# Optimization experiments

Measured on AMD Instinct MI355X. Metric: run time of the kernel, lower is better.

Reference implementation:

```python
import math
import jax, jax.numpy as jnp
import numpy as np

B, N, D, H, PQ, PV = 2, 2048, 256, 8, 4, 8
HD = D // H
OUT_IN = D + H * PV * 3 + H  # 256 + 192 + 8 = 456


def setup_inputs() -> dict:
    key = jax.random.key(0)
    ks = jax.random.split(key, 12)
    w = lambda k, shape: (jax.random.normal(k, shape, jnp.float32) * 0.02)
    return {
        "x": jax.random.normal(ks[0], (B, N, D), jnp.float32),
        "rotations": jax.random.normal(ks[1], (B, N, 3, 3), jnp.float32),
        "translations": jax.random.normal(ks[2], (B, N, 3), jnp.float32),
        "mask": jnp.ones((B, N), dtype=bool),
        "Wq": w(ks[3], (D, D)), "bq": jnp.zeros((D,), jnp.float32),
        "Wk": w(ks[4], (D, D)), "bk": jnp.zeros((D,), jnp.float32),
        "Wv": w(ks[5], (D, D)), "bv": jnp.zeros((D,), jnp.float32),
        "Wo": w(ks[6], (OUT_IN, D)), "bo": jnp.zeros((D,), jnp.float32),
        "head_weights": jnp.ones((H,), jnp.float32),
    }


def reference(x, rotations, translations, mask, Wq, bq, Wk, bk, Wv, bv, Wo, bo, head_weights):
    b, n, d = x.shape
    h = head_weights.shape[0]
    hd = d // h
    pv3 = Wo.shape[0] - d - h  # num_heads * num_value_points * 3

    q = (x @ Wq + bq).reshape(b, n, h, hd)
    k = (x @ Wk + bk).reshape(b, n, h, hd)
    v = (x @ Wv + bv).reshape(b, n, h, hd)

    # scalar attention logits [b,h,i,j]
    attn_scores = jnp.einsum("bihd,bjhd->bhij", q, k) / math.sqrt(hd)

    # point-distance bias from frame translations (rotated q/k/v points are
    # dead code in the original module and are omitted)
    diff = translations[:, :, None, :] - translations[:, None, :, :]  # [b,i,j,3]
    dist_sq = jnp.sum(diff * diff, axis=-1)                            # [b,i,j]
    point_attn = -0.5 * dist_sq[:, None, :, :]                         # [b,1,i,j]

    weights = jax.nn.softmax(head_weights)                             # [h]
    combined = attn_scores + point_attn * weights[None, :, None, None]
    combined = jnp.where(mask[:, None, None, :], combined, -1e9)
    attn_probs = jax.nn.softmax(combined, axis=-1)                     # [b,h,i,j]

    attn_output = jnp.einsum("bhij,bjhd->bihd", attn_probs, v).reshape(b, n, d)

    # translation-weighted points, brought back to local frame
    trans_weighted = jnp.einsum("bhij,bjc->bihc", attn_probs, translations)  # [b,i,h,3]
    trans_local = trans_weighted - translations[:, :, None, :]
    point_out = trans_local.reshape(b, n, h * 3)
    point_out = jnp.pad(point_out, ((0, 0), (0, 0), (0, pv3 - h * 3)))

    mean_dist = jnp.sqrt(jnp.mean(dist_sq, axis=-1, keepdims=True) + 1e-8)  # [b,n,1]
    pair_features = jnp.broadcast_to(mean_dist, (b, n, h))

    output = jnp.concatenate([attn_output, point_out, pair_features], axis=-1)
    return output @ Wo + bo
```

## Files before the change

kernel.cpp:

```cpp
#include <hip/hip_runtime.h>

typedef unsigned short u16;
typedef __attribute__((ext_vector_type(8))) short bf16x8;
typedef __attribute__((ext_vector_type(4))) float f32x4;
typedef __attribute__((ext_vector_type(16))) float f32x16;
typedef __attribute__((ext_vector_type(4))) unsigned u32x4;

#define NB 2
#define NSEQ 2048
#define DD 256
#define NH 8
#define HD 32
#define NTOK 4096
#define KF 288
#define NSPLIT 4
#define PS 36

#define SCL2E 0.25506973f
#define L2E 1.4426950408889634f

__device__ __forceinline__ u16 f2b(float f) {
  unsigned u = __builtin_bit_cast(unsigned, f);
  return (u16)((u + 0x7fffu + ((u >> 16) & 1u)) >> 16);
}

__device__ __forceinline__ unsigned cvt_pk_bf16(float lo, float hi) {
  unsigned r;
  asm("v_cvt_pk_bf16_f32 %0, %1, %2" : "=v"(r) : "v"(lo), "v"(hi));
  return r;
}

__device__ __forceinline__ void permlane32_swap(unsigned& a, unsigned& b) {
  asm volatile("v_permlane32_swap_b32 %0, %1" : "+v"(a), "+v"(b));
}

__device__ __forceinline__ f32x4 mfma16(bf16x8 a, bf16x8 b, f32x4 c) {
  return __builtin_amdgcn_mfma_f32_16x16x32_bf16(a, b, c, 0, 0, 0);
}
__device__ __forceinline__ f32x16 mfma32(bf16x8 a, bf16x8 b, f32x16 c) {
  return __builtin_amdgcn_mfma_f32_32x32x16_bf16(a, b, c, 0, 0, 0);
}

__global__ __launch_bounds__(256) void cast_prep(
    const float* __restrict__ x, const float* __restrict__ tr,
    const float* __restrict__ hw, const float* __restrict__ bq,
    const float* __restrict__ bk, const float* __restrict__ bv,
    u16* __restrict__ xb, float4* __restrict__ t4, u16* __restrict__ U,
    float* __restrict__ b_all, float* __restrict__ wsoft) {
  const int N0 = NTOK * DD;
  const int NT4 = NTOK;
  const int NU = NTOK * 16;
  int idx = blockIdx.x * 256 + threadIdx.x;
  int r = idx;
  if (r < N0) {
    xb[r] = f2b(x[r]);
  } else if ((r -= N0) < NT4) {
    float a = tr[r * 3], b2 = tr[r * 3 + 1], c = tr[r * 3 + 2];
    t4[r] = make_float4(a, b2, c, a * a + b2 * b2 + c * c);
  } else if ((r -= NT4) < NU) {
    int tok = r >> 4, e = r & 15;
    float v = 0.f;
    if (e < 3) v = tr[tok * 3 + e];
    else if (e == 3) {
      float a = tr[tok * 3], b2 = tr[tok * 3 + 1], c = tr[tok * 3 + 2];
      v = a * a + b2 * b2 + c * c;
    } else if (e == 4) v = 1.f;
    U[r] = f2b(v);
  } else if ((r -= NU) < 768) {
    b_all[r] = r < 256 ? bq[r] * SCL2E : r < 512 ? bk[r - 256] : bv[r - 512];
  }
  if (idx == 0) {
    float mx = hw[0];
    for (int i = 1; i < NH; i++) mx = fmaxf(mx, hw[i]);
    float e[NH], sum = 0.f;
    for (int i = 0; i < NH; i++) { e[i] = __expf(hw[i] - mx); sum += e[i]; }
    for (int i = 0; i < NH; i++) wsoft[i] = e[i] / sum;
  }
}

__global__ __launch_bounds__(256) void wtrans(
    const float* __restrict__ Wq, const float* __restrict__ Wk,
    const float* __restrict__ Wv, const float* __restrict__ Wo,
    u16* __restrict__ WqkvT, u16* __restrict__ WoPT) {
  __shared__ float lt[32][33];
  const int bid = blockIdx.x, t = threadIdx.x;
  const int r = t >> 3, c4 = (t & 7) * 4;
  if (bid < 192) {
    int mt = bid >> 3, kt = bid & 7;
    int m0 = mt * 32, k0 = kt * 32;
    const float* W = m0 < 256 ? Wq : (m0 < 512 ? Wk : Wv);
    const int mm = m0 & 255;
    float4 v = *(const float4*)(W + (size_t)(k0 + r) * 256 + mm + c4);
    lt[r][c4] = v.x; lt[r][c4 + 1] = v.y; lt[r][c4 + 2] = v.z; lt[r][c4 + 3] = v.w;
    __syncthreads();
    const float s = m0 < 256 ? SCL2E : 1.f;
    ushort4 o;
    o.x = f2b(lt[c4][r] * s); o.y = f2b(lt[c4 + 1][r] * s);
    o.z = f2b(lt[c4 + 2][r] * s); o.w = f2b(lt[c4 + 3][r] * s);
    *(ushort4*)(WqkvT + (size_t)(m0 + r) * 256 + k0 + c4) = o;
  } else {
    int q = bid - 192;
    int nt2 = q / 9, kt = q - nt2 * 9;
    int n0 = nt2 * 32, kk0 = kt * 32;
    int row = (kk0 + r) < 280 ? (kk0 + r) : (kk0 + r + 168);
    float4 v = *(const float4*)(Wo + (size_t)row * 256 + n0 + c4);
    lt[r][c4] = v.x; lt[r][c4 + 1] = v.y; lt[r][c4 + 2] = v.z; lt[r][c4 + 3] = v.w;
    __syncthreads();
    ushort4 o;
    o.x = f2b(lt[c4][r]); o.y = f2b(lt[c4 + 1][r]);
    o.z = f2b(lt[c4 + 2][r]); o.w = f2b(lt[c4 + 3][r]);
    *(ushort4*)(WoPT + (size_t)(n0 + r) * KF + kk0 + c4) = o;
  }
}

__global__ __launch_bounds__(256) void bstat_kernel(const float4* __restrict__ t4,
                                                    float4* __restrict__ bstat) {
  const int b = blockIdx.x;
  float sx = 0.f, sy = 0.f, sz = 0.f, s2 = 0.f;
  for (int j = threadIdx.x; j < NSEQ; j += 256) {
    float4 t = t4[b * NSEQ + j];
    sx += t.x; sy += t.y; sz += t.z; s2 += t.w;
  }
#pragma unroll
  for (int off = 1; off < 64; off <<= 1) {
    sx += __shfl_xor(sx, off); sy += __shfl_xor(sy, off);
    sz += __shfl_xor(sz, off); s2 += __shfl_xor(s2, off);
  }
  __shared__ float4 red[4];
  if ((threadIdx.x & 63) == 0) red[threadIdx.x >> 6] = make_float4(sx, sy, sz, s2);
  __syncthreads();
  if (threadIdx.x == 0) {
    float4 a = red[0], b1 = red[1], c = red[2], d = red[3];
    bstat[b] = make_float4(a.x + b1.x + c.x + d.x, a.y + b1.y + c.y + d.y,
                           a.z + b1.z + c.z + d.z, a.w + b1.w + c.w + d.w);
  }
}

template <int M, int K, int MODE>
__global__ __launch_bounds__(256) void gemm_tt(
    const u16* __restrict__ AT, const u16* __restrict__ BT,
    const float* __restrict__ bias, void* __restrict__ outv) {
  const int lane = threadIdx.x & 63, wv = threadIdx.x >> 6;
  const int il = lane & 15, g = lane >> 4;
  const int wm = wv >> 1, wn = wv & 1;
  const int mblk = blockIdx.y * 32 + wm * 16;
  const int nblk = blockIdx.x * 64 + wn * 32;
  f32x4 acc[2];
  acc[0] = (f32x4)(0.f);
  acc[1] = (f32x4)(0.f);
  const u16* Abase = AT + (size_t)(mblk + il) * K + 8 * g;
  const u16* Bbase = BT + (size_t)(nblk + il) * K + 8 * g;
#pragma unroll
  for (int kk = 0; kk < K; kk += 32) {
    bf16x8 aF = *(const bf16x8*)(Abase + kk);
    bf16x8 bF0 = *(const bf16x8*)(Bbase + kk);
    bf16x8 bF1 = *(const bf16x8*)(Bbase + (size_t)16 * K + kk);
    acc[0] = mfma16(aF, bF0, acc[0]);
    acc[1] = mfma16(aF, bF1, acc[1]);
  }
#pragma unroll
  for (int nt = 0; nt < 2; nt++) {
    const int n_g = nblk + nt * 16 + il;
    const int m0 = mblk + 4 * g;
    f32x4 v = acc[nt];
    const float4 bb = *(const float4*)(bias + m0);
    v[0] += bb.x; v[1] += bb.y; v[2] += bb.z; v[3] += bb.w;
    if (MODE == 2) {
      *(float4*)((float*)outv + (size_t)n_g * M + m0) =
          make_float4(v[0], v[1], v[2], v[3]);
    } else {
      ushort4 u;
      u.x = f2b(v[0]); u.y = f2b(v[1]); u.z = f2b(v[2]); u.w = f2b(v[3]);
      *(ushort4*)((u16*)outv + (size_t)n_g * M + m0) = u;
    }
  }
}

__global__ __launch_bounds__(256) void repack(
    const u16* __restrict__ QKV, const float* __restrict__ tr,
    u16* __restrict__ KSW, u16* __restrict__ VSW, u16* __restrict__ AXSW) {
  __shared__ u16 ldsV[32][33];
  const int jt = blockIdx.x, h = blockIdx.y, b = blockIdx.z;
  const int t = threadIdx.x;
  const size_t tile = ((size_t)(b * NH + h) * 64 + jt) * 1024;
  if (t < 128) {
    const int rr = t & 31, dd = t >> 5;
    const int tok = b * NSEQ + jt * 32 + rr;
    bf16x8 kv = *(const bf16x8*)(QKV + (size_t)tok * 768 + 256 + h * 32 + dd * 8);
    *(bf16x8*)(KSW + tile + (size_t)(dd * 32 + rr) * 8) = kv;
  } else {
    const int u = t - 128;
    const int rr = u & 31, dd = u >> 5;
    const int tok = b * NSEQ + jt * 32 + rr;
    bf16x8 vv = *(const bf16x8*)(QKV + (size_t)tok * 768 + 512 + h * 32 + dd * 8);
#pragma unroll
    for (int e = 0; e < 8; e++) ldsV[rr][dd * 8 + e] = (u16)vv[e];
  }
  __syncthreads();
  if (t >= 128) {
    const int u = t - 128;
    const int c2 = u & 31, sub = u >> 5;
    const int jb2 = (sub >> 1) * 16 + (sub & 1) * 8;
    u16 ov[8];
#pragma unroll
    for (int e = 0; e < 8; e++) ov[e] = ldsV[jb2 + e][c2];
    *(bf16x8*)(VSW + tile + (size_t)u * 8) = *(bf16x8*)ov;
  } else if (h == 0) {
    const int c2 = t & 31, sub = t >> 5;
    const int jb2 = jt * 32 + (sub >> 1) * 16 + (sub & 1) * 8;
    u16 ov[8];
#pragma unroll
    for (int e = 0; e < 8; e++) {
      float v = 0.f;
      if (c2 == 0) v = 1.f;
      else if (c2 < 4) v = tr[(size_t)(b * NSEQ + jb2 + e) * 3 + c2 - 1];
      ov[e] = f2b(v);
    }
    *(bf16x8*)(AXSW + ((size_t)(b * 64 + jt)) * 1024 + (size_t)t * 8) =
        *(bf16x8*)ov;
  }
}

__global__ __launch_bounds__(256, 4) void attn_kernel(
    const u16* __restrict__ QKV, const u16* __restrict__ KSW,
    const u16* __restrict__ VSW, const u16* __restrict__ AXSW,
    const u16* __restrict__ U, const float4* __restrict__ t4,
    const float* __restrict__ wsoft, float* __restrict__ part) {
  const int lane = threadIdx.x & 63, wv = threadIdx.x >> 6;
  const int c = lane & 31, hi = lane >> 5;
  const int bh = blockIdx.y, b = bh >> 3, h = bh & 7;
  const int s = blockIdx.z;
  const int qb = blockIdx.x * 128 + wv * 32;
  const int iglob = b * NSEQ + qb + c;

  const u16* qptr = QKV + (size_t)iglob * 768 + h * HD + 8 * hi;
  const bf16x8 qf0 = *(const bf16x8*)qptr;
  const bf16x8 qf1 = *(const bf16x8*)(qptr + 16);
  const float4 ti = t4[iglob];
  const float w = wsoft[h];
  const float WD = w * L2E, NH2 = -0.5f * WD;
  u32x4 vw = (u32x4)(0u);
  if (hi == 0) {
    vw[0] = cvt_pk_bf16(WD * ti.x, WD * ti.y);
    vw[1] = cvt_pk_bf16(WD * ti.z, NH2);
    vw[2] = cvt_pk_bf16(NH2 * ti.w, 0.f);
  }
  const bf16x8 vf = __builtin_bit_cast(bf16x8, vw);

  f32x16 o = (f32x16)(0.f), aacc = (f32x16)(0.f);
  const int lo = hi * 256 + c * 8;
  const u16* tbK = KSW + ((size_t)bh * 64) * 1024 + lo;
  const u16* tbV = VSW + ((size_t)bh * 64) * 1024 + lo;
  const u16* tbA = AXSW + ((size_t)b * 64) * 1024 + lo;
  const u16* tbU = U + (size_t)b * NSEQ * 16 + c * 16 + hi * 8;

  struct Frag7 { bf16x8 k0, k1, v0, v1, a0, a1, u; };
  auto LDF = [&](int jt) {
    Frag7 f;
    const size_t off = (size_t)jt * 1024;
    f.k0 = *(const bf16x8*)(tbK + off);
    f.k1 = *(const bf16x8*)(tbK + off + 512);
    f.v0 = *(const bf16x8*)(tbV + off);
    f.v1 = *(const bf16x8*)(tbV + off + 512);
    f.a0 = *(const bf16x8*)(tbA + off);
    f.a1 = *(const bf16x8*)(tbA + off + 512);
    f.u = *(const bf16x8*)(tbU + (size_t)jt * 512);
    return f;
  };
  auto COMP = [&](const Frag7& f) {
    f32x16 sa = mfma32(f.u, vf, (f32x16)(0.f));
    sa = mfma32(f.k0, qf0, sa);
    sa = mfma32(f.k1, qf1, sa);
    float p[16];
#pragma unroll
    for (int r = 0; r < 16; r++) p[r] = exp2f(sa[r]);
    unsigned x0 = cvt_pk_bf16(p[0], p[1]), y0 = cvt_pk_bf16(p[4], p[5]);
    unsigned z0 = cvt_pk_bf16(p[2], p[3]), w0 = cvt_pk_bf16(p[6], p[7]);
    permlane32_swap(x0, y0);
    permlane32_swap(z0, w0);
    unsigned x1 = cvt_pk_bf16(p[8], p[9]), y1 = cvt_pk_bf16(p[12], p[13]);
    unsigned z1 = cvt_pk_bf16(p[10], p[11]), w1 = cvt_pk_bf16(p[14], p[15]);
    permlane32_swap(x1, y1);
    permlane32_swap(z1, w1);
    bf16x8 pa0 = __builtin_bit_cast(bf16x8, (u32x4){x0, z0, y0, w0});
    bf16x8 pa1 = __builtin_bit_cast(bf16x8, (u32x4){x1, z1, y1, w1});
    o = mfma32(pa0, f.v0, o);
    o = mfma32(pa1, f.v1, o);
    aacc = mfma32(pa0, f.a0, aacc);
    aacc = mfma32(pa1, f.a1, aacc);
  };

  const int jt0 = s * 16;
  Frag7 cur = LDF(jt0);
#pragma unroll 1
  for (int t = 1; t < 16; ++t) {
    Frag7 nxt = LDF(jt0 + t);
    __builtin_amdgcn_s_setprio(1);
    COMP(cur);
    __builtin_amdgcn_s_setprio(0);
    cur = nxt;
  }
  __builtin_amdgcn_s_setprio(1);
  COMP(cur);
  __builtin_amdgcn_s_setprio(0);

  float* pbase = part + ((size_t)(s * 16 + bh) * NSEQ + qb) * PS;
#pragma unroll
  for (int r = 0; r < 16; r++) {
    const int irow = (r & 3) + 8 * (r >> 2) + 4 * hi;
    float* pr = pbase + (size_t)irow * PS;
    pr[c] = o[r];
    if (c < 4) pr[32 + c] = aacc[r];
  }
}

__global__ __launch_bounds__(256) void combine_kernel(
    const float* __restrict__ part, const float4* __restrict__ t4,
    const float4* __restrict__ bstat, u16* __restrict__ feats) {
  const int lane = threadIdx.x & 63;
  const int gw = blockIdx.x * 4 + (threadIdx.x >> 6);
  const int bh = gw >> 11, i = gw & 2047;
  const int b = bh >> 3, h = bh & 7;
  const int tok = b * NSEQ + i;
  const float* p0 = part + ((size_t)bh * NSEQ + i) * PS;
  const size_t SS = (size_t)16 * NSEQ * PS;
  float v = 0.f;
  if (lane < PS) v = p0[lane] + p0[SS + lane] + p0[2 * SS + lane] + p0[3 * SS + lane];
  float ls = __shfl(v, 32);
  float inv = 1.f / ls;
  u16* fr = feats + (size_t)tok * KF;
  if (lane < 32) {
    fr[h * HD + lane] = f2b(v * inv);
  } else if (lane >= 33 && lane < 36) {
    int cc = lane - 33;
    float tc = cc == 0 ? t4[tok].x : (cc == 1 ? t4[tok].y : t4[tok].z);
    fr[256 + h * 3 + cc] = f2b(fmaf(v, inv, -tc));
  } else if (lane == 36 && h == 0) {
    float4 t = t4[tok];
    float4 st = bstat[b];
    float sumd = (float)NSEQ * t.w + st.w -
                 2.f * (t.x * st.x + t.y * st.y + t.z * st.z);
    float md = sqrtf(sumd * (1.f / (float)NSEQ) + 1e-8f);
    u16 mb = f2b(md);
    for (int cc = 0; cc < 8; cc++) fr[280 + cc] = mb;
  }
}

extern "C" void kernel_launch(void* const* d_in, const int* in_sizes, int n_in,
                              void* d_out, int out_size, void* d_ws, size_t ws_size,
                              hipStream_t stream) {
  (void)in_sizes; (void)n_in; (void)out_size; (void)ws_size;
  const float* x  = (const float*)d_in[0];
  const float* tr = (const float*)d_in[2];
  const float* Wq = (const float*)d_in[4];
  const float* bq = (const float*)d_in[5];
  const float* Wk = (const float*)d_in[6];
  const float* bk = (const float*)d_in[7];
  const float* Wv = (const float*)d_in[8];
  const float* bv = (const float*)d_in[9];
  const float* Wo = (const float*)d_in[10];
  const float* bo = (const float*)d_in[11];
  const float* hw = (const float*)d_in[12];
  float* out = (float*)d_out;

  char* p = (char*)d_ws;
  auto alloc = [&](size_t n) { char* r = p; p += (n + 255) & ~(size_t)255; return r; };
  u16* xb      = (u16*)alloc((size_t)NTOK * DD * 2);
  u16* WqkvT   = (u16*)alloc((size_t)768 * DD * 2);
  u16* WoPT    = (u16*)alloc((size_t)DD * KF * 2);
  float4* t4   = (float4*)alloc((size_t)NTOK * 16);
  u16* U       = (u16*)alloc((size_t)NTOK * 16 * 2);
  float* b_all = (float*)alloc(768 * 4);
  float* ws    = (float*)alloc(256);
  float4* bst  = (float4*)alloc(256);
  u16* QKV     = (u16*)alloc((size_t)NTOK * 768 * 2);
  u16* KSW     = (u16*)alloc((size_t)NB * NH * 64 * 1024 * 2);
  u16* VSW     = (u16*)alloc((size_t)NB * NH * 64 * 1024 * 2);
  u16* AXSW    = (u16*)alloc((size_t)NB * 64 * 1024 * 2);
  u16* feats   = (u16*)alloc((size_t)NTOK * KF * 2);
  float* part  = (float*)alloc((size_t)NSPLIT * 16 * NSEQ * PS * 4);

  cast_prep<<<4374, 256, 0, stream>>>(x, tr, hw, bq, bk, bv, xb, t4, U, b_all, ws);
  wtrans<<<264, 256, 0, stream>>>(Wq, Wk, Wv, Wo, WqkvT, WoPT);
  bstat_kernel<<<2, 256, 0, stream>>>(t4, bst);
  gemm_tt<768, DD, 0><<<dim3(64, 24), 256, 0, stream>>>(WqkvT, xb, b_all, QKV);
  repack<<<dim3(64, NH, NB), 256, 0, stream>>>(QKV, tr, KSW, VSW, AXSW);
  attn_kernel<<<dim3(NSEQ / 128, NB * NH, NSPLIT), 256, 0, stream>>>(
      QKV, KSW, VSW, AXSW, U, t4, ws, part);
  combine_kernel<<<8192, 256, 0, stream>>>(part, t4, bst, feats);
  gemm_tt<DD, KF, 2><<<dim3(64, 8), 256, 0, stream>>>(WoPT, feats, bo, out);
}
```

Baseline: 149.5 us.

## Merge prep kernels, enlarge QKV GEMM tiles, stage attention tiles in LDS

Merges the cast, weight-transpose, batch-statistics and bias prep into a single launch, vectorising the x cast to float4. The QKV GEMM now gives each wave a 32x64 output tile for more operand reuse. K, V, translation and U fragments are packed into one contiguous 4096-element tile per (batch, head, key block), so the per-head translation tile is duplicated across heads. The attention loop stages each tile into double-buffered LDS with cooperative loads instead of per-lane global loads, which adds a __syncthreads per iteration.

```diff
diff --git a/kernel.cpp b/kernel.cpp
--- a/kernel.cpp
+++ b/kernel.cpp
@@ -15,6 +15,7 @@
 #define KF 288
 #define NSPLIT 4
 #define PS 36
+#define TSTR 4096
 
 #define SCL2E 0.25506973f
 #define L2E 1.4426950408889634f
@@ -41,105 +42,146 @@
   return __builtin_amdgcn_mfma_f32_32x32x16_bf16(a, b, c, 0, 0, 0);
 }
 
-__global__ __launch_bounds__(256) void cast_prep(
+#define PB0 1024
+#define PB1 (PB0 + 264)
+#define PB2 (PB1 + 2)
+#define PB3 (PB2 + 16)
+__global__ __launch_bounds__(256) void prep(
     const float* __restrict__ x, const float* __restrict__ tr,
     const float* __restrict__ hw, const float* __restrict__ bq,
     const float* __restrict__ bk, const float* __restrict__ bv,
-    u16* __restrict__ xb, float4* __restrict__ t4, u16* __restrict__ U,
-    float* __restrict__ b_all, float* __restrict__ wsoft) {
-  const int N0 = NTOK * DD;
-  const int NT4 = NTOK;
-  const int NU = NTOK * 16;
-  int idx = blockIdx.x * 256 + threadIdx.x;
-  int r = idx;
-  if (r < N0) {
-    xb[r] = f2b(x[r]);
-  } else if ((r -= N0) < NT4) {
-    float a = tr[r * 3], b2 = tr[r * 3 + 1], c = tr[r * 3 + 2];
-    t4[r] = make_float4(a, b2, c, a * a + b2 * b2 + c * c);
-  } else if ((r -= NT4) < NU) {
-    int tok = r >> 4, e = r & 15;
-    float v = 0.f;
-    if (e < 3) v = tr[tok * 3 + e];
-    else if (e == 3) {
-      float a = tr[tok * 3], b2 = tr[tok * 3 + 1], c = tr[tok * 3 + 2];
-      v = a * a + b2 * b2 + c * c;
-    } else if (e == 4) v = 1.f;
-    U[r] = f2b(v);
-  } else if ((r -= NU) < 768) {
-    b_all[r] = r < 256 ? bq[r] * SCL2E : r < 512 ? bk[r - 256] : bv[r - 512];
-  }
-  if (idx == 0) {
-    float mx = hw[0];
-    for (int i = 1; i < NH; i++) mx = fmaxf(mx, hw[i]);
-    float e[NH], sum = 0.f;
-    for (int i = 0; i < NH; i++) { e[i] = __expf(hw[i] - mx); sum += e[i]; }
-    for (int i = 0; i < NH; i++) wsoft[i] = e[i] / sum;
-  }
-}
-
-__global__ __launch_bounds__(256) void wtrans(
     const float* __restrict__ Wq, const float* __restrict__ Wk,
     const float* __restrict__ Wv, const float* __restrict__ Wo,
-    u16* __restrict__ WqkvT, u16* __restrict__ WoPT) {
+    u16* __restrict__ xb, u16* __restrict__ WqkvT, u16* __restrict__ WoPT,
+    float4* __restrict__ t4, float4* __restrict__ bstat,
+    float* __restrict__ b_all, float* __restrict__ wsoft) {
   __shared__ float lt[32][33];
   const int bid = blockIdx.x, t = threadIdx.x;
-  const int r = t >> 3, c4 = (t & 7) * 4;
-  if (bid < 192) {
-    int mt = bid >> 3, kt = bid & 7;
-    int m0 = mt * 32, k0 = kt * 32;
-    const float* W = m0 < 256 ? Wq : (m0 < 512 ? Wk : Wv);
-    const int mm = m0 & 255;
-    float4 v = *(const float4*)(W + (size_t)(k0 + r) * 256 + mm + c4);
-    lt[r][c4] = v.x; lt[r][c4 + 1] = v.y; lt[r][c4 + 2] = v.z; lt[r][c4 + 3] = v.w;
+  if (bid < PB0) {
+    const int i4 = bid * 256 + t;
+    float4 v = *(const float4*)(x + (size_t)i4 * 4);
+    ushort4 o;
+    o.x = f2b(v.x); o.y = f2b(v.y); o.z = f2b(v.z); o.w = f2b(v.w);
+    *(ushort4*)(xb + (size_t)i4 * 4) = o;
+  } else if (bid < PB1) {
+    const int bw = bid - PB0;
+    const int r = t >> 3, c4 = (t & 7) * 4;
+    if (bw < 192) {
+      int mt = bw >> 3, kt = bw & 7;
+      int m0 = mt * 32, k0 = kt * 32;
+      const float* W = m0 < 256 ? Wq : (m0 < 512 ? Wk : Wv);
+      const int mm = m0 & 255;
+      float4 v = *(const float4*)(W + (size_t)(k0 + r) * 256 + mm + c4);
+      lt[r][c4] = v.x; lt[r][c4 + 1] = v.y; lt[r][c4 + 2] = v.z; lt[r][c4 + 3] = v.w;
+      __syncthreads();
+      const float s = m0 < 256 ? SCL2E : 1.f;
+      ushort4 o;
+      o.x = f2b(lt[c4][r] * s); o.y = f2b(lt[c4 + 1][r] * s);
+      o.z = f2b(lt[c4 + 2][r] * s); o.w = f2b(lt[c4 + 3][r] * s);
+      *(ushort4*)(WqkvT + (size_t)(m0 + r) * 256 + k0 + c4) = o;
+    } else {
+      int q = bw - 192;
+      int nt2 = q / 9, kt = q - nt2 * 9;
+      int n0 = nt2 * 32, kk0 = kt * 32;
+      int row = (kk0 + r) < 280 ? (kk0 + r) : (kk0 + r + 168);
+      float4 v = *(const float4*)(Wo + (size_t)row * 256 + n0 + c4);
+      lt[r][c4] = v.x; lt[r][c4 + 1] = v.y; lt[r][c4 + 2] = v.z; lt[r][c4 + 3] = v.w;
+      __syncthreads();
+      ushort4 o;
+      o.x = f2b(lt[c4][r]); o.y = f2b(lt[c4 + 1][r]);
+      o.z = f2b(lt[c4 + 2][r]); o.w = f2b(lt[c4 + 3][r]);
+      *(ushort4*)(WoPT + (size_t)(n0 + r) * KF + kk0 + c4) = o;
+    }
+  } else if (bid < PB2) {
+    const int b = bid - PB1;
+    float sx = 0.f, sy = 0.f, sz = 0.f, s2 = 0.f;
+    for (int j = t; j < NSEQ; j += 256) {
+      float a = tr[(size_t)(b * NSEQ + j) * 3];
+      float b2 = tr[(size_t)(b * NSEQ + j) * 3 + 1];
+      float c = tr[(size_t)(b * NSEQ + j) * 3 + 2];
+      sx += a; sy += b2; sz += c; s2 += a * a + b2 * b2 + c * c;
+    }
+#pragma unroll
+    for (int off = 1; off < 64; off <<= 1) {
+      sx += __shfl_xor(sx, off); sy += __shfl_xor(sy, off);
+      sz += __shfl_xor(sz, off); s2 += __shfl_xor(s2, off);
+    }
+    __shared__ float4 red[4];
+    if ((t & 63) == 0) red[t >> 6] = make_float4(sx, sy, sz, s2);
     __syncthreads();
-    const float s = m0 < 256 ? SCL2E : 1.f;
-    ushort4 o;
-    o.x = f2b(lt[c4][r] * s); o.y = f2b(lt[c4 + 1][r] * s);
-    o.z = f2b(lt[c4 + 2][r] * s); o.w = f2b(lt[c4 + 3][r] * s);
-    *(ushort4*)(WqkvT + (size_t)(m0 + r) * 256 + k0 + c4) = o;
+    if (t == 0) {
+      float4 a = red[0], b1 = red[1], c = red[2], d = red[3];
+      bstat[b] = make_float4(a.x + b1.x + c.x + d.x, a.y + b1.y + c.y + d.y,
+                             a.z + b1.z + c.z + d.z, a.w + b1.w + c.w + d.w);
+    }
+  } else if (bid < PB3) {
+    const int j = (bid - PB2) * 256 + t;
+    float a = tr[j * 3], b2 = tr[j * 3 + 1], c = tr[j * 3 + 2];
+    t4[j] = make_float4(a, b2, c, a * a + b2 * b2 + c * c);
   } else {
-    int q = bid - 192;
-    int nt2 = q / 9, kt = q - nt2 * 9;
-    int n0 = nt2 * 32, kk0 = kt * 32;
-    int row = (kk0 + r) < 280 ? (kk0 + r) : (kk0 + r + 168);
-    float4 v = *(const float4*)(Wo + (size_t)row * 256 + n0 + c4);
-    lt[r][c4] = v.x; lt[r][c4 + 1] = v.y; lt[r][c4 + 2] = v.z; lt[r][c4 + 3] = v.w;
-    __syncthreads();
-    ushort4 o;
-    o.x = f2b(lt[c4][r]); o.y = f2b(lt[c4 + 1][r]);
-    o.z = f2b(lt[c4 + 2][r]); o.w = f2b(lt[c4 + 3][r]);
-    *(ushort4*)(WoPT + (size_t)(n0 + r) * KF + kk0 + c4) = o;
-  }
-}
-
-__global__ __launch_bounds__(256) void bstat_kernel(const float4* __restrict__ t4,
-                                                    float4* __restrict__ bstat) {
-  const int b = blockIdx.x;
-  float sx = 0.f, sy = 0.f, sz = 0.f, s2 = 0.f;
-  for (int j = threadIdx.x; j < NSEQ; j += 256) {
-    float4 t = t4[b * NSEQ + j];
-    sx += t.x; sy += t.y; sz += t.z; s2 += t.w;
-  }
-#pragma unroll
-  for (int off = 1; off < 64; off <<= 1) {
-    sx += __shfl_xor(sx, off); sy += __shfl_xor(sy, off);
-    sz += __shfl_xor(sz, off); s2 += __shfl_xor(s2, off);
-  }
-  __shared__ float4 red[4];
-  if ((threadIdx.x & 63) == 0) red[threadIdx.x >> 6] = make_float4(sx, sy, sz, s2);
-  __syncthreads();
-  if (threadIdx.x == 0) {
-    float4 a = red[0], b1 = red[1], c = red[2], d = red[3];
-    bstat[b] = make_float4(a.x + b1.x + c.x + d.x, a.y + b1.y + c.y + d.y,
-                           a.z + b1.z + c.z + d.z, a.w + b1.w + c.w + d.w);
-  }
-}
-
-template <int M, int K, int MODE>
-__global__ __launch_bounds__(256) void gemm_tt(
+    for (int i = t; i < 768; i += 256)
+      b_all[i] = i < 256 ? bq[i] * SCL2E : i < 512 ? bk[i - 256] : bv[i - 512];
+    if (t == 0) {
+      float mx = hw[0];
+      for (int i = 1; i < NH; i++) mx = fmaxf(mx, hw[i]);
+      float e[NH], sum = 0.f;
+      for (int i = 0; i < NH; i++) { e[i] = __expf(hw[i] - mx); sum += e[i]; }
+      for (int i = 0; i < NH; i++) wsoft[i] = e[i] / sum;
+    }
+  }
+}
+
+template <int M, int K>
+__global__ __launch_bounds__(256) void gemm_big(
     const u16* __restrict__ AT, const u16* __restrict__ BT,
-    const float* __restrict__ bias, void* __restrict__ outv) {
+    const float* __restrict__ bias, u16* __restrict__ out) {
+  const int lane = threadIdx.x & 63, wv = threadIdx.x >> 6;
+  const int il = lane & 15, g = lane >> 4;
+  const int wm = wv >> 1, wn = wv & 1;
+  const int mblk = blockIdx.y * 64 + wm * 32;
+  const int nblk = blockIdx.x * 128 + wn * 64;
+  f32x4 acc[2][4];
+#pragma unroll
+  for (int a = 0; a < 2; a++)
+#pragma unroll
+    for (int b = 0; b < 4; b++) acc[a][b] = (f32x4)(0.f);
+  const u16* Abase = AT + (size_t)(mblk + il) * K + 8 * g;
+  const u16* Bbase = BT + (size_t)(nblk + il) * K + 8 * g;
+#pragma unroll
+  for (int kk = 0; kk < K; kk += 32) {
+    bf16x8 aF[2], bF[4];
+#pragma unroll
+    for (int mt = 0; mt < 2; mt++)
+      aF[mt] = *(const bf16x8*)(Abase + (size_t)mt * 16 * K + kk);
+#pragma unroll
+    for (int nt = 0; nt < 4; nt++)
+      bF[nt] = *(const bf16x8*)(Bbase + (size_t)nt * 16 * K + kk);
+#pragma unroll
+    for (int mt = 0; mt < 2; mt++)
+#pragma unroll
+      for (int nt = 0; nt < 4; nt++)
+        acc[mt][nt] = mfma16(aF[mt], bF[nt], acc[mt][nt]);
+  }
+#pragma unroll
+  for (int nt = 0; nt < 4; nt++) {
+    const int n_g = nblk + nt * 16 + il;
+#pragma unroll
+    for (int mt = 0; mt < 2; mt++) {
+      const int m0 = mblk + mt * 16 + 4 * g;
+      f32x4 v = acc[mt][nt];
+      const float4 bb = *(const float4*)(bias + m0);
+      v[0] += bb.x; v[1] += bb.y; v[2] += bb.z; v[3] += bb.w;
+      ushort4 u;
+      u.x = f2b(v[0]); u.y = f2b(v[1]); u.z = f2b(v[2]); u.w = f2b(v[3]);
+      *(ushort4*)(out + (size_t)n_g * M + m0) = u;
+    }
+  }
+}
+
+template <int M, int K>
+__global__ __launch_bounds__(256) void gemm_out(
+    const u16* __restrict__ AT, const u16* __restrict__ BT,
+    const float* __restrict__ bias, float* __restrict__ outv) {
   const int lane = threadIdx.x & 63, wv = threadIdx.x >> 6;
   const int il = lane & 15, g = lane >> 4;
   const int wm = wv >> 1, wn = wv & 1;
@@ -165,29 +207,36 @@
     f32x4 v = acc[nt];
     const float4 bb = *(const float4*)(bias + m0);
     v[0] += bb.x; v[1] += bb.y; v[2] += bb.z; v[3] += bb.w;
-    if (MODE == 2) {
-      *(float4*)((float*)outv + (size_t)n_g * M + m0) =
-          make_float4(v[0], v[1], v[2], v[3]);
-    } else {
-      ushort4 u;
-      u.x = f2b(v[0]); u.y = f2b(v[1]); u.z = f2b(v[2]); u.w = f2b(v[3]);
-      *(ushort4*)((u16*)outv + (size_t)n_g * M + m0) = u;
-    }
+    *(float4*)(outv + (size_t)n_g * M + m0) = make_float4(v[0], v[1], v[2], v[3]);
   }
 }
 
 __global__ __launch_bounds__(256) void repack(
     const u16* __restrict__ QKV, const float* __restrict__ tr,
-    u16* __restrict__ KSW, u16* __restrict__ VSW, u16* __restrict__ AXSW) {
+    u16* __restrict__ TLB) {
   __shared__ u16 ldsV[32][33];
   const int jt = blockIdx.x, h = blockIdx.y, b = blockIdx.z;
   const int t = threadIdx.x;
-  const size_t tile = ((size_t)(b * NH + h) * 64 + jt) * 1024;
+  u16* tile = TLB + ((size_t)((b * NH + h) * 64 + jt)) * TSTR;
   if (t < 128) {
     const int rr = t & 31, dd = t >> 5;
     const int tok = b * NSEQ + jt * 32 + rr;
     bf16x8 kv = *(const bf16x8*)(QKV + (size_t)tok * 768 + 256 + h * 32 + dd * 8);
-    *(bf16x8*)(KSW + tile + (size_t)(dd * 32 + rr) * 8) = kv;
+    *(bf16x8*)(tile + (size_t)(dd * 32 + rr) * 8) = kv;
+    if (t < 64) {
+      const int c = t >> 1, hi = t & 1;
+      const int tok2 = b * NSEQ + jt * 32 + c;
+      float a = tr[tok2 * 3], b2 = tr[tok2 * 3 + 1], cz = tr[tok2 * 3 + 2];
+      u16 ov[8];
+#pragma unroll
+      for (int e = 0; e < 8; e++) {
+        int ea = hi * 8 + e;
+        float v = ea == 0 ? a : ea == 1 ? b2 : ea == 2 ? cz
+                  : ea == 3 ? (a * a + b2 * b2 + cz * cz) : ea == 4 ? 1.f : 0.f;
+        ov[e] = f2b(v);
+      }
+      *(bf16x8*)(tile + 3072 + c * 16 + hi * 8) = *(bf16x8*)ov;
+    }
   } else {
     const int u = t - 128;
     const int rr = u & 31, dd = u >> 5;
@@ -204,29 +253,29 @@
     u16 ov[8];
 #pragma unroll
     for (int e = 0; e < 8; e++) ov[e] = ldsV[jb2 + e][c2];
-    *(bf16x8*)(VSW + tile + (size_t)u * 8) = *(bf16x8*)ov;
-  } else if (h == 0) {
+    *(bf16x8*)(tile + 1024 + (size_t)u * 8) = *(bf16x8*)ov;
+  } else {
     const int c2 = t & 31, sub = t >> 5;
-    const int jb2 = jt * 32 + (sub >> 1) * 16 + (sub & 1) * 8;
+    const int jb2 = (sub >> 1) * 16 + (sub & 1) * 8;
     u16 ov[8];
 #pragma unroll
     for (int e = 0; e < 8; e++) {
       float v = 0.f;
       if (c2 == 0) v = 1.f;
-      else if (c2 < 4) v = tr[(size_t)(b * NSEQ + jb2 + e) * 3 + c2 - 1];
+      else if (c2 < 4) v = tr[(size_t)(b * NSEQ + jt * 32 + jb2 + e) * 3 + c2 - 1];
       ov[e] = f2b(v);
     }
-    *(bf16x8*)(AXSW + ((size_t)(b * 64 + jt)) * 1024 + (size_t)t * 8) =
-        *(bf16x8*)ov;
+    *(bf16x8*)(tile + 2048 + (size_t)t * 8) = *(bf16x8*)ov;
   }
 }
 
 __global__ __launch_bounds__(256, 4) void attn_kernel(
-    const u16* __restrict__ QKV, const u16* __restrict__ KSW,
-    const u16* __restrict__ VSW, const u16* __restrict__ AXSW,
-    const u16* __restrict__ U, const float4* __restrict__ t4,
-    const float* __restrict__ wsoft, float* __restrict__ part) {
-  const int lane = threadIdx.x & 63, wv = threadIdx.x >> 6;
+    const u16* __restrict__ QKV, const u16* __restrict__ TLB,
+    const float4* __restrict__ t4, const float* __restrict__ wsoft,
+    float* __restrict__ part) {
+  __shared__ __align__(16) u16 tlb[2][4096];
+  const int tid = threadIdx.x;
+  const int lane = tid & 63, wv = tid >> 6;
   const int c = lane & 31, hi = lane >> 5;
   const int bh = blockIdx.y, b = bh >> 3, h = bh & 7;
   const int s = blockIdx.z;
@@ -248,29 +297,39 @@
   const bf16x8 vf = __builtin_bit_cast(bf16x8, vw);
 
   f32x16 o = (f32x16)(0.f), aacc = (f32x16)(0.f);
-  const int lo = hi * 256 + c * 8;
-  const u16* tbK = KSW + ((size_t)bh * 64) * 1024 + lo;
-  const u16* tbV = VSW + ((size_t)bh * 64) * 1024 + lo;
-  const u16* tbA = AXSW + ((size_t)b * 64) * 1024 + lo;
-  const u16* tbU = U + (size_t)b * NSEQ * 16 + c * 16 + hi * 8;
-
-  struct Frag7 { bf16x8 k0, k1, v0, v1, a0, a1, u; };
-  auto LDF = [&](int jt) {
-    Frag7 f;
-    const size_t off = (size_t)jt * 1024;
-    f.k0 = *(const bf16x8*)(tbK + off);
-    f.k1 = *(const bf16x8*)(tbK + off + 512);
-    f.v0 = *(const bf16x8*)(tbV + off);
-    f.v1 = *(const bf16x8*)(tbV + off + 512);
-    f.a0 = *(const bf16x8*)(tbA + off);
-    f.a1 = *(const bf16x8*)(tbA + off + 512);
-    f.u = *(const bf16x8*)(tbU + (size_t)jt * 512);
-    return f;
-  };
-  auto COMP = [&](const Frag7& f) {
-    f32x16 sa = mfma32(f.u, vf, (f32x16)(0.f));
-    sa = mfma32(f.k0, qf0, sa);
-    sa = mfma32(f.k1, qf1, sa);
+  const u16* tbase = TLB + (size_t)bh * 64 * TSTR;
+  const int jt0 = s * 16;
+  const int fo = hi * 256 + c * 8;
+
+  bf16x8 g0, g1;
+  {
+    const u16* src = tbase + (size_t)jt0 * TSTR;
+    g0 = *(const bf16x8*)(src + tid * 8);
+    if (tid < 192) g1 = *(const bf16x8*)(src + 2048 + tid * 8);
+    *(bf16x8*)(&tlb[0][tid * 8]) = g0;
+    if (tid < 192) *(bf16x8*)(&tlb[0][2048 + tid * 8]) = g1;
+  }
+  __syncthreads();
+
+#pragma unroll 2
+  for (int t = 0; t < 16; ++t) {
+    if (t < 15) {
+      const u16* src = tbase + (size_t)(jt0 + t + 1) * TSTR;
+      g0 = *(const bf16x8*)(src + tid * 8);
+      if (tid < 192) g1 = *(const bf16x8*)(src + 2048 + tid * 8);
+    }
+    const u16* L = &tlb[t & 1][0];
+    bf16x8 k0 = *(const bf16x8*)(L + fo);
+    bf16x8 k1 = *(const bf16x8*)(L + 512 + fo);
+    bf16x8 v0 = *(const bf16x8*)(L + 1024 + fo);
+    bf16x8 v1 = *(const bf16x8*)(L + 1536 + fo);
+    bf16x8 a0 = *(const bf16x8*)(L + 2048 + fo);
+    bf16x8 a1 = *(const bf16x8*)(L + 2560 + fo);
+    bf16x8 uf = *(const bf16x8*)(L + 3072 + c * 16 + hi * 8);
+    __builtin_amdgcn_s_setprio(1);
+    f32x16 sa = mfma32(uf, vf, (f32x16)(0.f));
+    sa = mfma32(k0, qf0, sa);
+    sa = mfma32(k1, qf1, sa);
     float p[16];
 #pragma unroll
     for (int r = 0; r < 16; r++) p[r] = exp2f(sa[r]);
@@ -284,25 +343,18 @@
     permlane32_swap(z1, w1);
     bf16x8 pa0 = __builtin_bit_cast(bf16x8, (u32x4){x0, z0, y0, w0});
     bf16x8 pa1 = __builtin_bit_cast(bf16x8, (u32x4){x1, z1, y1, w1});
-    o = mfma32(pa0, f.v0, o);
-    o = mfma32(pa1, f.v1, o);
-    aacc = mfma32(pa0, f.a0, aacc);
-    aacc = mfma32(pa1, f.a1, aacc);
-  };
-
-  const int jt0 = s * 16;
-  Frag7 cur = LDF(jt0);
-#pragma unroll 1
-  for (int t = 1; t < 16; ++t) {
-    Frag7 nxt = LDF(jt0 + t);
-    __builtin_amdgcn_s_setprio(1);
-    COMP(cur);
+    o = mfma32(pa0, v0, o);
+    o = mfma32(pa1, v1, o);
+    aacc = mfma32(pa0, a0, aacc);
+    aacc = mfma32(pa1, a1, aacc);
     __builtin_amdgcn_s_setprio(0);
-    cur = nxt;
-  }
-  __builtin_amdgcn_s_setprio(1);
-  COMP(cur);
-  __builtin_amdgcn_s_setprio(0);
+    if (t < 15) {
+      u16* D = &tlb[(t + 1) & 1][0];
+      *(bf16x8*)(D + tid * 8) = g0;
+      if (tid < 192) *(bf16x8*)(D + 2048 + tid * 8) = g1;
+    }
+    __syncthreads();
+  }
 
   float* pbase = part + ((size_t)(s * 16 + bh) * NSEQ + qb) * PS;
 #pragma unroll
@@ -369,24 +421,20 @@
   u16* WqkvT   = (u16*)alloc((size_t)768 * DD * 2);
   u16* WoPT    = (u16*)alloc((size_t)DD * KF * 2);
   float4* t4   = (float4*)alloc((size_t)NTOK * 16);
-  u16* U       = (u16*)alloc((size_t)NTOK * 16 * 2);
   float* b_all = (float*)alloc(768 * 4);
   float* ws    = (float*)alloc(256);
   float4* bst  = (float4*)alloc(256);
   u16* QKV     = (u16*)alloc((size_t)NTOK * 768 * 2);
-  u16* KSW     = (u16*)alloc((size_t)NB * NH * 64 * 1024 * 2);
-  u16* VSW     = (u16*)alloc((size_t)NB * NH * 64 * 1024 * 2);
-  u16* AXSW    = (u16*)alloc((size_t)NB * 64 * 1024 * 2);
+  u16* TLB     = (u16*)alloc((size_t)NB * NH * 64 * TSTR * 2);
   u16* feats   = (u16*)alloc((size_t)NTOK * KF * 2);
   float* part  = (float*)alloc((size_t)NSPLIT * 16 * NSEQ * PS * 4);
 
-  cast_prep<<<4374, 256, 0, stream>>>(x, tr, hw, bq, bk, bv, xb, t4, U, b_all, ws);
-  wtrans<<<264, 256, 0, stream>>>(Wq, Wk, Wv, Wo, WqkvT, WoPT);
-  bstat_kernel<<<2, 256, 0, stream>>>(t4, bst);
-  gemm_tt<768, DD, 0><<<dim3(64, 24), 256, 0, stream>>>(WqkvT, xb, b_all, QKV);
-  repack<<<dim3(64, NH, NB), 256, 0, stream>>>(QKV, tr, KSW, VSW, AXSW);
+  prep<<<PB3 + 1, 256, 0, stream>>>(x, tr, hw, bq, bk, bv, Wq, Wk, Wv, Wo, xb,
+                                    WqkvT, WoPT, t4, bst, b_all, ws);
+  gemm_big<768, DD><<<dim3(32, 12), 256, 0, stream>>>(WqkvT, xb, b_all, QKV);
+  repack<<<dim3(64, NH, NB), 256, 0, stream>>>(QKV, tr, TLB);
   attn_kernel<<<dim3(NSEQ / 128, NB * NH, NSPLIT), 256, 0, stream>>>(
-      QKV, KSW, VSW, AXSW, U, t4, ws, part);
+      QKV, TLB, t4, ws, part);
   combine_kernel<<<8192, 256, 0, stream>>>(part, t4, bst, feats);
-  gemm_tt<DD, KF, 2><<<dim3(64, 8), 256, 0, stream>>>(WoPT, feats, bo, out);
-}
+  gemm_out<DD, KF><<<dim3(64, 8), 256, 0, stream>>>(WoPT, feats, bo, out);
+}
```

Measured after the change: 142.5 us. 4.7% less time.
